# Kernel optimization log

Measured on AMD Instinct MI355X. Metric: run time of the kernel, lower is better.

## Reference

```python
import jax, jax.numpy as jnp
import numpy as np

B, S, H, NH = 4, 2048, 1024, 16
DK = H // NH


def setup_inputs() -> dict:
    key = jax.random.key(0)
    ks = jax.random.split(key, 12)
    sd = 1.0 / np.sqrt(H)
    inp = {
        "query": jax.random.normal(ks[0], (B, S, H), jnp.float32),
        "key_": jax.random.normal(ks[1], (B, S, H), jnp.float32),
        "value": jax.random.normal(ks[2], (B, S, H), jnp.float32),
        "mask": jax.random.randint(ks[3], (B, 1, S, S), 0, 2) == 1,
        "Wq": jax.random.uniform(ks[4], (H, H), jnp.float32, -sd, sd),
        "bq": jnp.zeros((H,), jnp.float32),
        "Wk": jax.random.uniform(ks[5], (H, H), jnp.float32, -sd, sd),
        "bk": jnp.zeros((H,), jnp.float32),
        "Wv": jax.random.uniform(ks[6], (H, H), jnp.float32, -sd, sd),
        "bv": jnp.zeros((H,), jnp.float32),
        "Wo": jax.random.uniform(ks[7], (H, H), jnp.float32, -sd, sd),
        "bo": jnp.zeros((H,), jnp.float32),
    }
    return inp


def reference(query, key_, value, mask, Wq, bq, Wk, bk, Wv, bv, Wo, bo):
    b = query.shape[0]
    # projections; nn.Linear computes x @ W^T + b
    q = (query @ Wq.T + bq).reshape(b, -1, NH, DK).transpose(0, 2, 1, 3)  # [B,NH,S,DK]
    k = (key_ @ Wk.T + bk).reshape(b, -1, NH, DK).transpose(0, 2, 1, 3)
    v = (value @ Wv.T + bv).reshape(b, -1, NH, DK).transpose(0, 2, 1, 3)
    scores = jnp.einsum("bhqd,bhkd->bhqk", q, k) / jnp.sqrt(jnp.float32(DK))
    min_val = jnp.finfo(scores.dtype).min
    scores = jnp.where(mask, min_val, scores)
    attn = jax.nn.softmax(scores, axis=-1)
    attn = jnp.where(mask, 0.0, attn)
    # dropout_rate = 0.0 -> identity
    x = jnp.einsum("bhqk,bhkd->bhqd", attn, v)
    x = x.transpose(0, 2, 1, 3).reshape(b, -1, NH * DK)  # [B,S,H]
    return x @ Wo.T + bo
```

## Files before the change

kernel.cpp:

```cpp
#include <hip/hip_runtime.h>
#include <hip/hip_bf16.h>
#include <stdint.h>

#define B_  4
#define S_  2048
#define H_  1024
#define NH_ 16
#define DK_ 64
#define M_  (B_*S_)

typedef unsigned short u16;
typedef __attribute__((ext_vector_type(8))) short bfrag;
typedef __attribute__((ext_vector_type(4))) float facc;
typedef __attribute__((ext_vector_type(16))) float f32x16;
typedef __attribute__((ext_vector_type(4))) unsigned int u32x4;
typedef __attribute__((ext_vector_type(2))) unsigned int u32x2;

__device__ __forceinline__ u16 f2bf(float f) {
  uint32_t u = __float_as_uint(f);
  return (u16)((u + 0x7fffu + ((u >> 16) & 1u)) >> 16);
}

__device__ __forceinline__ uint32_t cvtpk_bf16(float a, float b) {
  uint32_t r;
  asm("v_cvt_pk_bf16_f32 %0, %1, %2" : "=v"(r) : "v"(a), "v"(b));
  return r;
}

__global__ __launch_bounds__(256) void prep_kernel(
    const float* __restrict__ qa, const float* __restrict__ ka, const float* __restrict__ va,
    const float* __restrict__ Wq, const float* __restrict__ Wk,
    const float* __restrict__ Wv, const float* __restrict__ Wo,
    const int* __restrict__ mask,
    u16* __restrict__ qo, u16* __restrict__ ko, u16* __restrict__ vo,
    u16* __restrict__ wqo, u16* __restrict__ wko, u16* __restrict__ wvo, u16* __restrict__ woo,
    uint32_t* __restrict__ mbytes, float qscale) {
  const int bid = blockIdx.x;
  const int tid = threadIdx.x;
  if (bid < 3072) {
    int seg = bid >> 10, sb = bid & 1023;
    const float* in = seg == 0 ? qa : seg == 1 ? ka : va;
    u16* out = seg == 0 ? qo : seg == 1 ? ko : vo;
    const int n4 = M_ * H_ / 4;
    for (int i = sb*256 + tid; i < n4; i += 1024*256) {
      float4 v = reinterpret_cast<const float4*>(in)[i];
      ushort4 o;
      o.x = f2bf(v.x); o.y = f2bf(v.y); o.z = f2bf(v.z); o.w = f2bf(v.w);
      reinterpret_cast<ushort4*>(out)[i] = o;
    }
  } else if (bid < 4096) {
    int seg = (bid - 3072) >> 8, sb = (bid - 3072) & 255;
    const float* in = seg == 0 ? Wq : seg == 1 ? Wk : seg == 2 ? Wv : Wo;
    u16* out = seg == 0 ? wqo : seg == 1 ? wko : seg == 2 ? wvo : woo;
    float sc = (seg == 0) ? qscale : 1.0f;
    const int n4 = H_ * H_ / 4;
    for (int i = sb*256 + tid; i < n4; i += 256*256) {
      float4 v = reinterpret_cast<const float4*>(in)[i];
      ushort4 o;
      o.x = f2bf(v.x * sc); o.y = f2bf(v.y * sc);
      o.z = f2bf(v.z * sc); o.w = f2bf(v.w * sc);
      reinterpret_cast<ushort4*>(out)[i] = o;
    }
  } else {
    int od = (bid - 4096)*256 + tid;
    int j = od & 7, l31q = (od >> 3) & 31, hl = (od >> 8) & 1;
    int wv_ = (od >> 9) & 3, c = (od >> 11) & 31, qblk = od >> 16;
    int bq = qblk*128 + wv_*32 + l31q;
    int4 v = *reinterpret_cast<const int4*>(mask + (size_t)bq*2048 + c*64 + 4*hl + 8*(j & 3) + 32*(j >> 2));
    uint32_t w = (v.x != 0 ? 1u : 0u) | (v.y != 0 ? 0x100u : 0u) |
                 (v.z != 0 ? 0x10000u : 0u) | (v.w != 0 ? 0x1000000u : 0u);
    mbytes[od] = w;
  }
}

#define GLD16(gsrc, ldst) \
  __builtin_amdgcn_global_load_lds((const __attribute__((address_space(1))) void*)(gsrc), \
                                   (__attribute__((address_space(3))) void*)(ldst), 16, 0, 0)

#define GEMM_KLOOP(A_, B_, As_, Bs_) \
  for (int k0 = 0; k0 < K; k0 += 64) { \
    const u16* Ab = (A_) + (size_t)m0 * K + k0; \
    const u16* Bb = (B_) + (size_t)n0 * K + k0; \
    _Pragma("unroll") \
    for (int i = 0; i < 4; i++) { \
      int idx = i*256 + tid; \
      int row = idx >> 3, q = idx & 7; \
      int qs = q ^ (row & 7); \
      char* la = (char*)(As_) + i*4096 + wave*1024; \
      char* lb = (char*)(Bs_) + i*4096 + wave*1024; \
      GLD16(Ab + (size_t)row*K + qs*8, la); \
      GLD16(Bb + (size_t)row*K + qs*8, lb); \
    } \
    __syncthreads(); \
    const int sa = (lo & 7) << 4; \
    _Pragma("unroll") \
    for (int kk = 0; kk < 2; kk++) { \
      bfrag af[4], bfv[4]; \
      _Pragma("unroll") \
      for (int t = 0; t < 4; t++) { \
        af[t]  = *reinterpret_cast<const bfrag*>((char*)(As_) + (wr*64 + t*16 + lo)*128 + ((kk*64 + hi*16) ^ sa)); \
        bfv[t] = *reinterpret_cast<const bfrag*>((char*)(Bs_) + (wc*64 + t*16 + lo)*128 + ((kk*64 + hi*16) ^ sa)); \
      } \
      _Pragma("unroll") \
      for (int mt = 0; mt < 4; mt++) \
        _Pragma("unroll") \
        for (int nt = 0; nt < 4; nt++) \
          acc[mt][nt] = __builtin_amdgcn_mfma_f32_16x16x32_bf16(af[mt], bfv[nt], acc[mt][nt], 0, 0, 0); \
    } \
    __syncthreads(); \
  }

__global__ __launch_bounds__(256) void qkv_gemm(const u16* __restrict__ qa, const u16* __restrict__ ka,
                                                const u16* __restrict__ va,
                                                const u16* __restrict__ Wqb, const u16* __restrict__ Wkb,
                                                const u16* __restrict__ Wvb,
                                                const float* __restrict__ bqp, const float* __restrict__ bkp,
                                                const float* __restrict__ bvp, float qbscale,
                                                u16* __restrict__ qh, u16* __restrict__ kh,
                                                u16* __restrict__ vt) {
  constexpr int K = H_;
  __shared__ __align__(16) u16 SH[2][128*64];
  u16* As = SH[0];
  u16* Bs = SH[1];
  const int tid = threadIdx.x;
  const int lane = tid & 63, wave = tid >> 6;
  const int lo = lane & 15, hi = lane >> 4;
  const int wr = wave >> 1, wc = wave & 1;
  const int wsel = blockIdx.y >> 3;
  const int m0 = blockIdx.x * 128, n0 = (blockIdx.y & 7) * 128;
  const u16* A  = wsel == 0 ? qa : wsel == 1 ? ka : va;
  const u16* Bm = wsel == 0 ? Wqb : wsel == 1 ? Wkb : Wvb;
  const float* bias = wsel == 0 ? bqp : wsel == 1 ? bkp : bvp;
  const float bscale = wsel == 0 ? qbscale : 1.0f;
  facc acc[4][4] = {};

  GEMM_KLOOP(A, Bm, As, Bs)

  if (wsel < 2) {
    u16* o = wsel == 0 ? qh : kh;
    #pragma unroll
    for (int nt = 0; nt < 4; nt++) {
      int n = n0 + wc*64 + nt*16 + lo;
      float bv = bias[n] * bscale;
      int hh = n >> 6, d = n & 63;
      #pragma unroll
      for (int mt = 0; mt < 4; mt++) {
        #pragma unroll
        for (int r = 0; r < 4; r++) {
          int m = m0 + wr*64 + mt*16 + hi*4 + r;
          int bb = m >> 11, s = m & (S_ - 1);
          o[(((size_t)bb*NH_ + hh)*S_ + s)*DK_ + d] = f2bf(acc[mt][nt][r] + bv);
        }
      }
    }
  } else {
    u16* scr = &SH[0][0];
    const int bb2 = m0 >> 11, s0r = m0 & (S_ - 1);
    #pragma unroll
    for (int p = 0; p < 2; p++) {
      __syncthreads();
      if (wc == p) {
        #pragma unroll
        for (int nt = 0; nt < 4; nt++) {
          int d = nt*16 + lo;
          float bv = bias[n0 + p*64 + d];
          #pragma unroll
          for (int mt = 0; mt < 4; mt++) {
            #pragma unroll
            for (int r = 0; r < 4; r++) {
              int s = wr*64 + mt*16 + hi*4 + r;
              *(u16*)((char*)scr + d*256 + ((s*2) ^ ((d & 7) << 4))) = f2bf(acc[mt][nt][r] + bv);
            }
          }
        }
      }
      __syncthreads();
      int hh = (n0 >> 6) + p;
      u16* vbase = vt + ((size_t)bb2*NH_ + hh) * DK_ * S_ + s0r;
      #pragma unroll
      for (int i = 0; i < 4; i++) {
        int idx = i*256 + tid;
        int d = idx >> 4, sc = idx & 15;
        bfrag v = *reinterpret_cast<const bfrag*>((char*)scr + d*256 + ((sc*16) ^ ((d & 7) << 4)));
        *reinterpret_cast<bfrag*>(vbase + (size_t)d*S_ + sc*8) = v;
      }
    }
  }
}

__global__ __launch_bounds__(256) void gemm_out(const u16* __restrict__ A, const u16* __restrict__ Bm,
                                                const float* __restrict__ bias, float* __restrict__ o) {
  constexpr int K = H_, N = H_;
  __shared__ __align__(16) u16 As[128*64];
  __shared__ __align__(16) u16 Bs[128*64];
  const int tid = threadIdx.x;
  const int lane = tid & 63, wave = tid >> 6;
  const int lo = lane & 15, hi = lane >> 4;
  const int wr = wave >> 1, wc = wave & 1;
  const int m0 = blockIdx.x * 128, n0 = blockIdx.y * 128;
  facc acc[4][4] = {};

  GEMM_KLOOP(A, Bm, As, Bs)

  #pragma unroll
  for (int nt = 0; nt < 4; nt++) {
    int n = n0 + wc*64 + nt*16 + lo;
    float bv = bias[n];
    #pragma unroll
    for (int mt = 0; mt < 4; mt++) {
      #pragma unroll
      for (int r = 0; r < 4; r++) {
        int m = m0 + wr*64 + mt*16 + hi*4 + r;
        o[(size_t)m*N + n] = acc[mt][nt][r] + bv;
      }
    }
  }
}

__global__ __launch_bounds__(256, 4) void attn_kernel(const u16* __restrict__ Qh, const u16* __restrict__ Kh,
                                                      const u16* __restrict__ Vt, const uint32_t* __restrict__ mbytes,
                                                      u16* __restrict__ xout) {
  __shared__ __align__(16) u16 Ks[2][64*64];
  __shared__ __align__(16) u16 Vs[2][64*64];
  const int tid = threadIdx.x;
  const int lane = tid & 63, wave = tid >> 6;
  const int l31 = lane & 31, hl = lane >> 5;
  const int gid = blockIdx.x;
  const int bh = (gid & 7) * 8 + (gid >> 7);
  const int qt = (gid >> 3) & 15;
  const int b = bh >> 4, hd = bh & 15;
  const int q0 = qt * 128;
  const size_t bhS = (size_t)bh * S_;
  const int swz = (lane & 7) << 4;

  bfrag qf[4];
  {
    const u16* qrow = Qh + (bhS + q0 + wave*32 + l31) * DK_;
    #pragma unroll
    for (int t = 0; t < 4; t++) qf[t] = *reinterpret_cast<const bfrag*>(qrow + t*16 + hl*8);
  }
  const int qblk = b*16 + qt;
  const char* mrowb = (const char*)mbytes + (size_t)qblk*262144 + wave*2048 + hl*1024 + l31*32;

  const int srow = wave*8 + (lane >> 3);
  const int scol = ((lane & 7) ^ (lane >> 3)) * 16;
  const char* ksrc = (const char*)(Kh + bhS * DK_) + (size_t)srow * 128 + scol;
  const char* vsrc = (const char*)(Vt + (size_t)bh * DK_ * S_) + (size_t)srow * (S_*2) + scol;

#define STAGE(buf, c) { \
    char* kl = (char*)Ks[buf] + wave*1024; \
    char* vl = (char*)Vs[buf] + wave*1024; \
    GLD16(ksrc + (size_t)(c)*8192,          kl); \
    GLD16(ksrc + (size_t)(c)*8192 + 4096,   kl + 4096); \
    GLD16(vsrc + (size_t)(c)*128,           vl); \
    GLD16(vsrc + (size_t)(c)*128 + 131072,  vl + 4096); \
  }

  float l_run = 0.f;
  f32x16 accO[2];
  #pragma unroll
  for (int e = 0; e < 16; e++) { accO[0][e] = 0.f; accO[1][e] = 0.f; }

  STAGE(0, 0);
  u32x4 mA_cur = *reinterpret_cast<const u32x4*>(mrowb);
  u32x4 mB_cur = *reinterpret_cast<const u32x4*>(mrowb + 16);
  __syncthreads();

  for (int c = 0; c < 32; c++) {
    const int cur = c & 1;
    if (c + 1 < 32) STAGE(cur ^ 1, c + 1);

    u32x4 mA = mA_cur, mB = mB_cur;
    if (c + 1 < 32) {
      const char* mn = mrowb + (size_t)(c + 1)*8192;
      mA_cur = *reinterpret_cast<const u32x4*>(mn);
      mB_cur = *reinterpret_cast<const u32x4*>(mn + 16);
    }

    f32x16 s0, s1;
    #pragma unroll
    for (int r = 0; r < 16; r++) {
      float f0 = (float)((mA[r >> 2] >> ((r & 3) * 8)) & 0xffu);
      float f1 = (float)((mB[r >> 2] >> ((r & 3) * 8)) & 0xffu);
      s0[r] = __builtin_fmaf(f0, -1e36f, -8.0f);
      s1[r] = __builtin_fmaf(f1, -1e36f, -8.0f);
    }

    const char* KsB = (const char*)Ks[cur];
    __builtin_amdgcn_s_setprio(1);
    #pragma unroll
    for (int t = 0; t < 4; t++) {
      bfrag k0 = *reinterpret_cast<const bfrag*>(KsB + l31*128        + ((t*32 + hl*16) ^ swz));
      bfrag k1 = *reinterpret_cast<const bfrag*>(KsB + (32 + l31)*128 + ((t*32 + hl*16) ^ swz));
      s0 = __builtin_amdgcn_mfma_f32_32x32x16_bf16(k0, qf[t], s0, 0, 0, 0);
      s1 = __builtin_amdgcn_mfma_f32_32x32x16_bf16(k1, qf[t], s1, 0, 0, 0);
    }
    __builtin_amdgcn_s_setprio(0);

    #pragma unroll
    for (int r = 0; r < 16; r++) {
      s0[r] = __builtin_amdgcn_exp2f(s0[r]);
      s1[r] = __builtin_amdgcn_exp2f(s1[r]);
    }
    float a8[8];
    #pragma unroll
    for (int r = 0; r < 8; r++) a8[r] = (s0[r] + s0[r+8]) + (s1[r] + s1[r+8]);
    l_run += ((a8[0] + a8[1]) + (a8[2] + a8[3])) + ((a8[4] + a8[5]) + (a8[6] + a8[7]));

    u32x4 pa[4];
    #pragma unroll
    for (int kt = 0; kt < 2; kt++) {
      uint32_t W[8];
      #pragma unroll
      for (int j = 0; j < 8; j++)
        W[j] = kt == 0 ? cvtpk_bf16(s0[2*j], s0[2*j+1]) : cvtpk_bf16(s1[2*j], s1[2*j+1]);
      u32x2 r02 = __builtin_amdgcn_permlane32_swap(W[0], W[2], false, false);
      u32x2 r13 = __builtin_amdgcn_permlane32_swap(W[1], W[3], false, false);
      u32x2 r46 = __builtin_amdgcn_permlane32_swap(W[4], W[6], false, false);
      u32x2 r57 = __builtin_amdgcn_permlane32_swap(W[5], W[7], false, false);
      pa[kt*2    ][0] = r02[0]; pa[kt*2    ][1] = r13[0]; pa[kt*2    ][2] = r02[1]; pa[kt*2    ][3] = r13[1];
      pa[kt*2 + 1][0] = r46[0]; pa[kt*2 + 1][1] = r57[0]; pa[kt*2 + 1][2] = r46[1]; pa[kt*2 + 1][3] = r57[1];
    }

    const char* VsB = (const char*)Vs[cur];
    __builtin_amdgcn_s_setprio(1);
    #pragma unroll
    for (int ks = 0; ks < 4; ks++) {
      bfrag pb = __builtin_bit_cast(bfrag, pa[ks]);
      bfrag v0 = *reinterpret_cast<const bfrag*>(VsB + l31*128        + ((ks*32 + hl*16) ^ swz));
      bfrag v1 = *reinterpret_cast<const bfrag*>(VsB + (32 + l31)*128 + ((ks*32 + hl*16) ^ swz));
      accO[0] = __builtin_amdgcn_mfma_f32_32x32x16_bf16(v0, pb, accO[0], 0, 0, 0);
      accO[1] = __builtin_amdgcn_mfma_f32_32x32x16_bf16(v1, pb, accO[1], 0, 0, 0);
    }
    __builtin_amdgcn_s_setprio(0);
    __syncthreads();
  }
#undef STAGE

  float l_tot = l_run + __shfl_xor(l_run, 32);
  float linv = (l_tot > 0.f) ? (1.f / l_tot) : 0.f;
  u16* Xs = (u16*)Ks;
  {
    char* xb = (char*)Xs + (wave*32 + l31) * 128;
    #pragma unroll
    for (int dt = 0; dt < 2; dt++)
      #pragma unroll
      for (int j = 0; j < 8; j++) {
        uint32_t w = cvtpk_bf16(accO[dt][2*j] * linv, accO[dt][2*j+1] * linv);
        int d = dt*32 + ((2*j) & 3) + 8*((2*j) >> 2) + 4*hl;
        *reinterpret_cast<uint32_t*>(xb + ((d*2) ^ swz)) = w;
      }
  }
  __syncthreads();
  {
    int row = tid >> 1, d0 = (tid & 1) * 32;
    int rsw = (row & 7) << 4;
    u16* orow = xout + ((size_t)b * S_ + q0 + row) * H_ + hd * DK_ + d0;
    #pragma unroll
    for (int i = 0; i < 4; i++) {
      bfrag v = *reinterpret_cast<const bfrag*>((char*)Xs + row*128 + ((d0*2 + i*16) ^ rsw));
      *reinterpret_cast<bfrag*>((char*)orow + i*16) = v;
    }
  }
}

extern "C" void kernel_launch(void* const* d_in, const int* in_sizes, int n_in,
                              void* d_out, int out_size, void* d_ws, size_t ws_size,
                              hipStream_t stream) {
  const float* query = (const float*)d_in[0];
  const float* key_  = (const float*)d_in[1];
  const float* value = (const float*)d_in[2];
  const int*   mask  = (const int*)d_in[3];
  const float* Wq = (const float*)d_in[4];
  const float* bq = (const float*)d_in[5];
  const float* Wk = (const float*)d_in[6];
  const float* bk = (const float*)d_in[7];
  const float* Wv = (const float*)d_in[8];
  const float* bv = (const float*)d_in[9];
  const float* Wo = (const float*)d_in[10];
  const float* bo = (const float*)d_in[11];
  float* out = (float*)d_out;

  char* ws = (char*)d_ws;
  const size_t MB = 1024 * 1024;
  u16* q_act = (u16*)(ws + 0*MB);
  u16* k_act = (u16*)(ws + 16*MB);
  u16* v_act = (u16*)(ws + 32*MB);
  u16* wq_b  = (u16*)(ws + 48*MB);
  u16* wk_b  = (u16*)(ws + 50*MB);
  u16* wv_b  = (u16*)(ws + 52*MB);
  u16* wo_b  = (u16*)(ws + 54*MB);
  u16* qh    = (u16*)(ws + 56*MB);
  u16* kh    = (u16*)(ws + 72*MB);
  u16* vt    = (u16*)(ws + 104*MB);
  u16* xb    = (u16*)(ws + 120*MB);
  uint32_t* mbytes = (uint32_t*)(ws + 136*MB);

  const float QSCALE = 0.125f * 1.44269504088896f;

  prep_kernel<<<20480, 256, 0, stream>>>(query, key_, value, Wq, Wk, Wv, Wo, mask,
                                         q_act, k_act, v_act, wq_b, wk_b, wv_b, wo_b,
                                         mbytes, QSCALE);

  qkv_gemm<<<dim3(M_/128, 24), 256, 0, stream>>>(q_act, k_act, v_act, wq_b, wk_b, wv_b,
                                                 bq, bk, bv, QSCALE, qh, kh, vt);
  attn_kernel<<<1024, 256, 0, stream>>>(qh, kh, vt, mbytes, xb);
  gemm_out<<<dim3(M_/128, H_/128), 256, 0, stream>>>(xb, wo_b, bo, out);
}
```

Measured before the change: 229.5 us.

## Fuse fp32-to-bf16 activation conversion into QKV GEMM tile loading

Removes the separate pass that converted the query, key and value activations to bf16 in the prep kernel. The QKV GEMM now loads fp32 activation tiles straight into LDS and converts them to bf16 with packed conversion instructions when building MFMA fragments. This avoids writing and re-reading three bf16 activation buffers. In exchange the A-tile LDS footprint doubles and the GEMM reads fp32 from global memory; the A tiles are reloaded once for each of the 8 n-blocks, and there is extra conversion ALU work in the inner loop.

```diff
diff --git a/kernel.cpp b/kernel.cpp
--- a/kernel.cpp
+++ b/kernel.cpp
@@ -28,28 +28,15 @@
 }
 
 __global__ __launch_bounds__(256) void prep_kernel(
-    const float* __restrict__ qa, const float* __restrict__ ka, const float* __restrict__ va,
     const float* __restrict__ Wq, const float* __restrict__ Wk,
     const float* __restrict__ Wv, const float* __restrict__ Wo,
     const int* __restrict__ mask,
-    u16* __restrict__ qo, u16* __restrict__ ko, u16* __restrict__ vo,
     u16* __restrict__ wqo, u16* __restrict__ wko, u16* __restrict__ wvo, u16* __restrict__ woo,
     uint32_t* __restrict__ mbytes, float qscale) {
   const int bid = blockIdx.x;
   const int tid = threadIdx.x;
-  if (bid < 3072) {
-    int seg = bid >> 10, sb = bid & 1023;
-    const float* in = seg == 0 ? qa : seg == 1 ? ka : va;
-    u16* out = seg == 0 ? qo : seg == 1 ? ko : vo;
-    const int n4 = M_ * H_ / 4;
-    for (int i = sb*256 + tid; i < n4; i += 1024*256) {
-      float4 v = reinterpret_cast<const float4*>(in)[i];
-      ushort4 o;
-      o.x = f2bf(v.x); o.y = f2bf(v.y); o.z = f2bf(v.z); o.w = f2bf(v.w);
-      reinterpret_cast<ushort4*>(out)[i] = o;
-    }
-  } else if (bid < 4096) {
-    int seg = (bid - 3072) >> 8, sb = (bid - 3072) & 255;
+  if (bid < 1024) {
+    int seg = bid >> 8, sb = bid & 255;
     const float* in = seg == 0 ? Wq : seg == 1 ? Wk : seg == 2 ? Wv : Wo;
     u16* out = seg == 0 ? wqo : seg == 1 ? wko : seg == 2 ? wvo : woo;
     float sc = (seg == 0) ? qscale : 1.0f;
@@ -62,7 +49,7 @@
       reinterpret_cast<ushort4*>(out)[i] = o;
     }
   } else {
-    int od = (bid - 4096)*256 + tid;
+    int od = (bid - 1024)*256 + tid;
     int j = od & 7, l31q = (od >> 3) & 31, hl = (od >> 8) & 1;
     int wv_ = (od >> 9) & 3, c = (od >> 11) & 31, qblk = od >> 16;
     int bq = qblk*128 + wv_*32 + l31q;
@@ -110,8 +97,8 @@
     __syncthreads(); \
   }
 
-__global__ __launch_bounds__(256) void qkv_gemm(const u16* __restrict__ qa, const u16* __restrict__ ka,
-                                                const u16* __restrict__ va,
+__global__ __launch_bounds__(256) void qkv_gemm(const float* __restrict__ qa, const float* __restrict__ ka,
+                                                const float* __restrict__ va,
                                                 const u16* __restrict__ Wqb, const u16* __restrict__ Wkb,
                                                 const u16* __restrict__ Wvb,
                                                 const float* __restrict__ bqp, const float* __restrict__ bkp,
@@ -119,22 +106,65 @@
                                                 u16* __restrict__ qh, u16* __restrict__ kh,
                                                 u16* __restrict__ vt) {
   constexpr int K = H_;
-  __shared__ __align__(16) u16 SH[2][128*64];
-  u16* As = SH[0];
-  u16* Bs = SH[1];
+  __shared__ __align__(16) float Asf[128*64];
+  __shared__ __align__(16) u16  Bs[128*64];
   const int tid = threadIdx.x;
   const int lane = tid & 63, wave = tid >> 6;
   const int lo = lane & 15, hi = lane >> 4;
   const int wr = wave >> 1, wc = wave & 1;
   const int wsel = blockIdx.y >> 3;
   const int m0 = blockIdx.x * 128, n0 = (blockIdx.y & 7) * 128;
-  const u16* A  = wsel == 0 ? qa : wsel == 1 ? ka : va;
+  const float* A = wsel == 0 ? qa : wsel == 1 ? ka : va;
   const u16* Bm = wsel == 0 ? Wqb : wsel == 1 ? Wkb : Wvb;
   const float* bias = wsel == 0 ? bqp : wsel == 1 ? bkp : bvp;
   const float bscale = wsel == 0 ? qbscale : 1.0f;
   facc acc[4][4] = {};
 
-  GEMM_KLOOP(A, Bm, As, Bs)
+  for (int k0 = 0; k0 < K; k0 += 64) {
+    const float* Ab = A + (size_t)m0 * K + k0;
+    const u16* Bb = Bm + (size_t)n0 * K + k0;
+    #pragma unroll
+    for (int i = 0; i < 8; i++) {
+      int idx = i*256 + tid;
+      int row = idx >> 4, q = idx & 15;
+      int qs = q ^ (row & 7);
+      char* la = (char*)Asf + i*4096 + wave*1024;
+      GLD16((const char*)(Ab + (size_t)row*K) + qs*16, la);
+    }
+    #pragma unroll
+    for (int i = 0; i < 4; i++) {
+      int idx = i*256 + tid;
+      int row = idx >> 3, q = idx & 7;
+      int qs = q ^ (row & 7);
+      char* lb = (char*)Bs + i*4096 + wave*1024;
+      GLD16(Bb + (size_t)row*K + qs*8, lb);
+    }
+    __syncthreads();
+    const int sa = (lo & 7) << 4;
+    const int s8 = lo & 7;
+    #pragma unroll
+    for (int kk = 0; kk < 2; kk++) {
+      bfrag af[4], bfv[4];
+      #pragma unroll
+      for (int t = 0; t < 4; t++) {
+        int ra = wr*64 + t*16 + lo;
+        const char* rowp = (const char*)Asf + ra*256;
+        float4 x = *reinterpret_cast<const float4*>(rowp + (((kk*8 + hi*2 + 0) ^ s8) * 16));
+        float4 y = *reinterpret_cast<const float4*>(rowp + (((kk*8 + hi*2 + 1) ^ s8) * 16));
+        u32x4 pk;
+        pk[0] = cvtpk_bf16(x.x, x.y); pk[1] = cvtpk_bf16(x.z, x.w);
+        pk[2] = cvtpk_bf16(y.x, y.y); pk[3] = cvtpk_bf16(y.z, y.w);
+        af[t] = __builtin_bit_cast(bfrag, pk);
+        bfv[t] = *reinterpret_cast<const bfrag*>((char*)Bs + (wc*64 + t*16 + lo)*128 + ((kk*64 + hi*16) ^ sa));
+      }
+      #pragma unroll
+      for (int mt = 0; mt < 4; mt++)
+        #pragma unroll
+        for (int nt = 0; nt < 4; nt++)
+          acc[mt][nt] = __builtin_amdgcn_mfma_f32_16x16x32_bf16(af[mt], bfv[nt], acc[mt][nt], 0, 0, 0);
+    }
+    __syncthreads();
+  }
 
   if (wsel < 2) {
     u16* o = wsel == 0 ? qh : kh;
@@ -154,7 +184,7 @@
       }
     }
   } else {
-    u16* scr = &SH[0][0];
+    u16* scr = (u16*)Asf;
     const int bb2 = m0 >> 11, s0r = m0 & (S_ - 1);
     #pragma unroll
     for (int p = 0; p < 2; p++) {
@@ -383,9 +413,6 @@
 
   char* ws = (char*)d_ws;
   const size_t MB = 1024 * 1024;
-  u16* q_act = (u16*)(ws + 0*MB);
-  u16* k_act = (u16*)(ws + 16*MB);
-  u16* v_act = (u16*)(ws + 32*MB);
   u16* wq_b  = (u16*)(ws + 48*MB);
   u16* wk_b  = (u16*)(ws + 50*MB);
   u16* wv_b  = (u16*)(ws + 52*MB);
@@ -398,11 +425,10 @@
 
   const float QSCALE = 0.125f * 1.44269504088896f;
 
-  prep_kernel<<<20480, 256, 0, stream>>>(query, key_, value, Wq, Wk, Wv, Wo, mask,
-                                         q_act, k_act, v_act, wq_b, wk_b, wv_b, wo_b,
-                                         mbytes, QSCALE);
-
-  qkv_gemm<<<dim3(M_/128, 24), 256, 0, stream>>>(q_act, k_act, v_act, wq_b, wk_b, wv_b,
+  prep_kernel<<<17408, 256, 0, stream>>>(Wq, Wk, Wv, Wo, mask,
+                                         wq_b, wk_b, wv_b, wo_b, mbytes, QSCALE);
+
+  qkv_gemm<<<dim3(M_/128, 24), 256, 0, stream>>>(query, key_, value, wq_b, wk_b, wv_b,
                                                  bq, bk, bv, QSCALE, qh, kh, vt);
   attn_kernel<<<1024, 256, 0, stream>>>(qh, kh, vt, mbytes, xb);
   gemm_out<<<dim3(M_/128, H_/128), 256, 0, stream>>>(xb, wo_b, bo, out);
```

Result: slower. 236.6 us (+3.1%).
